# Kernel optimization log

Measured on AMD Instinct MI355X. Metric: run time of the kernel, lower is better.

## Reference

```python
import jax, jax.numpy as jnp
import numpy as np

KS = (7, 7)
ST = (3, 3)
PD = (3, 3)
DIM = 512
HID = 1960  # 40 * 49, divisible by kernel_shape


def _patch_flat_idx(out_h, out_w):
    kh, kw = KS; sh, sw = ST; ph, pw = PD
    oh = (out_h + 2 * ph - kh) // sh + 1
    ow = (out_w + 2 * pw - kw) // sw + 1
    Wp = out_w + 2 * pw
    iy = jnp.arange(kh)[:, None, None, None] + (jnp.arange(oh) * sh)[None, None, :, None]
    ix = jnp.arange(kw)[None, :, None, None] + (jnp.arange(ow) * sw)[None, None, None, :]
    # (kh, kw, oh, ow) flat index into padded image
    return (iy * Wp + ix), oh, ow


def fold(patches, out_h, out_w):
    # patches: (B, C*kh*kw, L) -> (B, C, out_h, out_w), overlap-add like F.fold
    kh, kw = KS; ph, pw = PD
    idx, oh, ow = _patch_flat_idx(out_h, out_w)
    B, CK, L = patches.shape
    C = CK // (kh * kw)
    Hp, Wp = out_h + 2 * ph, out_w + 2 * pw
    p = patches.reshape(B, C, kh, kw, oh, ow)
    out = jnp.zeros((B, C, Hp * Wp), patches.dtype)
    out = out.at[:, :, idx.reshape(-1)].add(p.reshape(B, C, -1))
    return out.reshape(B, C, Hp, Wp)[:, :, ph:ph + out_h, pw:pw + out_w]


def unfold(img, out_h, out_w):
    # img: (B, C, H, W) -> (B, C*kh*kw, L), like F.unfold
    kh, kw = KS; ph, pw = PD
    idx, oh, ow = _patch_flat_idx(out_h, out_w)
    B, C = img.shape[:2]
    imgp = jnp.pad(img, ((0, 0), (0, 0), (ph, ph), (pw, pw)))
    flat = imgp.reshape(B, C, -1)
    g = flat[:, :, idx.reshape(-1)].reshape(B, C, kh, kw, oh, ow)
    return g.reshape(B, C * kh * kw, oh * ow)


def setup_inputs() -> dict:
    key = jax.random.key(0)
    k1, k2, k3, k4, k5 = jax.random.split(key, 5)
    x = jax.random.normal(k1, (2, 5760, DIM), dtype=jnp.float32)
    W1 = jax.random.normal(k2, (HID, DIM), dtype=jnp.float32) * 0.02
    b1 = jax.random.normal(k3, (HID,), dtype=jnp.float32) * 0.02
    W2 = jax.random.normal(k4, (DIM, HID), dtype=jnp.float32) * 0.02
    b2 = jax.random.normal(k5, (DIM,), dtype=jnp.float32) * 0.02
    return {"x": x, "W1": W1, "b1": b1, "W2": W2, "b2": b2, "out_h": 60, "out_w": 108}


def reference(x, W1, b1, W2, b2, out_h, out_w):
    kh, kw = KS; sh, sw = ST; ph, pw = PD
    oh = (out_h + 2 * ph - kh) // sh + 1
    ow = (out_w + 2 * pw - kw) // sw + 1
    n_vecs = oh * ow
    h = jnp.einsum('bnd,hd->bnh', x, W1) + b1          # (b, n, HID)
    b_, n, c = h.shape
    p = h.reshape(-1, n_vecs, c).transpose(0, 2, 1)     # (B', c, L)
    folded = fold(p, out_h, out_w)                      # (B', c//49, H, W)
    ones = jnp.ones((p.shape[0], kh * kw, n_vecs), h.dtype)
    norm = fold(ones, out_h, out_w)                     # (B', 1, H, W)
    y = unfold(folded / norm, out_h, out_w)             # (B', c, L)
    y = y.transpose(0, 2, 1).reshape(b_, n, c)
    out = jnp.einsum('bnh,dh->bnd', jax.nn.gelu(y, approximate=False), W2) + b2
    return out
```

## Files before the change

### kernel.cpp

```cpp
#include <hip/hip_runtime.h>
#include <cmath>

#define M_ROWS   11520
#define DIM      512
#define HID      1960
#define HIDP     2048
#define KP2      1984
#define OH       20
#define OW       36
#define LVEC     720
#define NCH      40
#define BPRIME   16

typedef unsigned short u16;
typedef __bf16 bf16x8 __attribute__((ext_vector_type(8)));
typedef float  f32x4  __attribute__((ext_vector_type(4)));
typedef unsigned short u16x8 __attribute__((ext_vector_type(8)));

__device__ __forceinline__ u16 f2bf(float f) {
    unsigned u = __float_as_uint(f);
    u += 0x7fffu + ((u >> 16) & 1u);
    return (u16)(u >> 16);
}
__device__ __forceinline__ float bf2f(u16 h) {
    return __uint_as_float(((unsigned)h) << 16);
}

__device__ __forceinline__ void gload_lds16(const void* g, void* l) {
    __builtin_amdgcn_global_load_lds(
        (const __attribute__((address_space(1))) void*)g,
        (__attribute__((address_space(3))) void*)l, 16, 0, 0);
}

#define CVT_XB   5760
#define CVT_W1B  1024
#define CVT_W2B  1024
#define CVT_Z    270
__global__ __launch_bounds__(256) void cvt_all(const float* __restrict__ x,
                                               const float* __restrict__ W1,
                                               const float* __restrict__ W2,
                                               u16* __restrict__ xb,
                                               u16* __restrict__ W1b,
                                               u16* __restrict__ W2b,
                                               u16* __restrict__ g2) {
    const int b = blockIdx.x;
    const int tid = threadIdx.x;
    ushort4 o;
    if (b < CVT_XB) {
        int i = (b * 256 + tid) * 4;
        float4 v = *(const float4*)(x + i);
        o.x = f2bf(v.x); o.y = f2bf(v.y); o.z = f2bf(v.z); o.w = f2bf(v.w);
        *(ushort4*)(xb + i) = o;
    } else if (b < CVT_XB + CVT_W1B) {
        int i = ((b - CVT_XB) * 256 + tid) * 4;
        if (i < HID * DIM) {
            float4 v = *(const float4*)(W1 + i);
            o.x = f2bf(v.x); o.y = f2bf(v.y); o.z = f2bf(v.z); o.w = f2bf(v.w);
        } else {
            o.x = o.y = o.z = o.w = 0;
        }
        *(ushort4*)(W1b + i) = o;
    } else if (b < CVT_XB + CVT_W1B + CVT_W2B) {
        int i = ((b - CVT_XB - CVT_W1B) * 256 + tid) * 4;
        int d = i / HIDP, c = i - d * HIDP;
        if (c < HID) {
            float4 v = *(const float4*)(W2 + (size_t)d * HID + c);
            o.x = f2bf(v.x); o.y = f2bf(v.y); o.z = f2bf(v.z); o.w = f2bf(v.w);
        } else {
            o.x = o.y = o.z = o.w = 0;
        }
        *(ushort4*)(W2b + i) = o;
    } else {
        int i = ((b - CVT_XB - CVT_W1B - CVT_W2B) * 256 + tid) * 4;
        int row = i / 24, c = i - row * 24;
        o.x = o.y = o.z = o.w = 0;
        *(ushort4*)(g2 + (size_t)row * HIDP + HID + c) = o;
    }
}

__global__ __launch_bounds__(1024, 8) void gemm1_k(const u16* __restrict__ A,
                                                   const u16* __restrict__ B,
                                                   const float* __restrict__ bias,
                                                   u16* __restrict__ C) {
    __shared__ u16 smem[128 * 136];
    u16* sA = smem;
    u16* sB = smem + 128 * 64;

    const int tid  = threadIdx.x;
    const int NB   = gridDim.x;
    const int v    = (blockIdx.x & 7) * (NB >> 3) + (blockIdx.x >> 3);
    const int bm   = v >> 4;
    const int bn   = v & 15;
    const int lane = tid & 63;
    const int wv   = tid >> 6;
    const int wm   = (wv >> 2) * 32;
    const int wn   = (wv & 3) * 32;
    const int r    = lane & 15;
    const int quad = lane >> 4;

    const size_t Arow0 = (size_t)bm * 128 * DIM;
    const size_t Brow0 = (size_t)bn * 128 * DIM;

    const int srow = tid >> 3;
    const int scg  = (tid & 7) ^ (srow & 7);

    f32x4 acc[2][2] = {};

    for (int kt = 0; kt < DIM; kt += 64) {
        __syncthreads();
        gload_lds16(A + Arow0 + (size_t)srow * DIM + kt + scg * 8, (char*)sA + tid * 16);
        gload_lds16(B + Brow0 + (size_t)srow * DIM + kt + scg * 8, (char*)sB + tid * 16);
        __syncthreads();
#pragma unroll
        for (int kk = 0; kk < 2; kk++) {
            bf16x8 af[2], bg[2];
#pragma unroll
            for (int m = 0; m < 2; m++) {
                int row = wm + m * 16 + r;
                int c   = (kk * 4 + quad) ^ (row & 7);
                af[m] = *(const bf16x8*)(sA + row * 64 + c * 8);
            }
#pragma unroll
            for (int u = 0; u < 2; u++) {
                int row = wn + u * 16 + r;
                int c   = (kk * 4 + quad) ^ (row & 7);
                bg[u] = *(const bf16x8*)(sB + row * 64 + c * 8);
            }
#pragma unroll
            for (int m = 0; m < 2; m++)
#pragma unroll
                for (int u = 0; u < 2; u++)
                    acc[m][u] = __builtin_amdgcn_mfma_f32_16x16x32_bf16(
                        af[m], bg[u], acc[m][u], 0, 0, 0);
        }
    }

    __syncthreads();
    const int gn0 = bn * 128;
#pragma unroll
    for (int u = 0; u < 2; u++) {
        int gnl = wn + u * 16 + r;
        int gng = gn0 + gnl;
        float bv = (gng < HID) ? bias[gng] : 0.0f;
#pragma unroll
        for (int m = 0; m < 2; m++) {
            int gml = wm + m * 16 + quad * 4;
#pragma unroll
            for (int q = 0; q < 4; q++)
                smem[(gml + q) * 136 + gnl] = f2bf(acc[m][u][q] + bv);
        }
    }
    __syncthreads();
    const int row = tid >> 3;
    const int seg = tid & 7;
    const u16* src = smem + row * 136 + seg * 16;
    u16* dst = C + (size_t)(bm * 128 + row) * HIDP + gn0 + seg * 16;
    *(u16x8*)dst       = *(const u16x8*)src;
    *(u16x8*)(dst + 8) = *(const u16x8*)(src + 8);
}

__global__ __launch_bounds__(512, 8) void gemm2_k(const u16* __restrict__ A,
                                                  const u16* __restrict__ B,
                                                  const float* __restrict__ bias,
                                                  float* __restrict__ C) {
    __shared__ u16 sA[128 * 64];
    __shared__ u16 sB[64 * 64];

    const int tid  = threadIdx.x;
    const int NB   = gridDim.x;
    const int v    = (blockIdx.x & 7) * (NB >> 3) + (blockIdx.x >> 3);
    const int bm   = v >> 3;
    const int bn   = v & 7;
    const int lane = tid & 63;
    const int wv   = tid >> 6;
    const int wm   = (wv >> 1) * 32;
    const int wn   = (wv & 1) * 32;
    const int r    = lane & 15;
    const int quad = lane >> 4;

    const size_t Arow0 = (size_t)bm * 128 * HIDP;
    const size_t Brow0 = (size_t)bn * 64 * HIDP;

    f32x4 acc[2][2] = {};

    for (int kt = 0; kt < KP2; kt += 64) {
        __syncthreads();
#pragma unroll
        for (int i = 0; i < 2; i++) {
            int e   = i * 512 + tid;
            int row = e >> 3;
            int cg  = (e & 7) ^ (row & 7);
            gload_lds16(A + Arow0 + (size_t)row * HIDP + kt + cg * 8, (char*)sA + e * 16);
        }
        {
            int row = tid >> 3;
            int cg  = (tid & 7) ^ (row & 7);
            gload_lds16(B + Brow0 + (size_t)row * HIDP + kt + cg * 8, (char*)sB + tid * 16);
        }
        __syncthreads();
#pragma unroll
        for (int kk = 0; kk < 2; kk++) {
            bf16x8 af[2], bg[2];
#pragma unroll
            for (int m = 0; m < 2; m++) {
                int row = wm + m * 16 + r;
                int c   = (kk * 4 + quad) ^ (row & 7);
                af[m] = *(const bf16x8*)(sA + row * 64 + c * 8);
            }
#pragma unroll
            for (int u = 0; u < 2; u++) {
                int row = wn + u * 16 + r;
                int c   = (kk * 4 + quad) ^ (row & 7);
                bg[u] = *(const bf16x8*)(sB + row * 64 + c * 8);
            }
#pragma unroll
            for (int m = 0; m < 2; m++)
#pragma unroll
                for (int u = 0; u < 2; u++)
                    acc[m][u] = __builtin_amdgcn_mfma_f32_16x16x32_bf16(
                        af[m], bg[u], acc[m][u], 0, 0, 0);
        }
    }

    const int gm0 = bm * 128 + wm;
    const int gn0 = bn * 64 + wn;
#pragma unroll
    for (int u = 0; u < 2; u++) {
        int gn = gn0 + u * 16 + r;
        float bv = bias[gn];
#pragma unroll
        for (int m = 0; m < 2; m++) {
            int gm = gm0 + m * 16 + quad * 4;
#pragma unroll
            for (int q = 0; q < 4; q++)
                C[(size_t)(gm + q) * DIM + gn] = acc[m][u][q] + bv;
        }
    }
}

__global__ __launch_bounds__(512) void mid_fused(const u16* __restrict__ hg,
                                                 u16* __restrict__ g2) {
    __shared__ u16 sh[12 * 20 * 56];
    __shared__ u16 sG[34 * 58];

    const int b   = blockIdx.x;
    const int bp  = b / (NCH * 4);
    const int rr  = b - bp * (NCH * 4);
    const int ch  = rr >> 2;
    const int s   = (rr >> 1) & 1;
    const int xh  = rr & 1;
    const int o0  = s * 10;
    const int lo  = s * 8;
    const int ox0 = xh * 16;
    const int n0  = bp * LVEC;
    const int c0  = ch * 49;
    const int c0f = c0 & ~7;
    const int koff = c0 & 7;
    const int tid = threadIdx.x;

    {
        const char* hb = (const char*)(hg + (size_t)(n0 + lo * 36 + ox0) * HIDP + c0f);
        for (int t = tid; t < 12 * 20 * 7; t += 512) {
            int r   = (int)(((unsigned)t * 74899u) >> 19);
            int c   = t - r * 7;
            int loy = (int)(((unsigned)r * 3277u) >> 16);
            int oxl = r - 20 * loy;
            gload_lds16(hb + (size_t)(loy * 36 + oxl) * (HIDP * 2) + c * 16,
                        (char*)sh + t * 16);
        }
    }
    __syncthreads();

    const int pxl = tid & 63;
    const int rg  = tid >> 6;
    if (pxl < 58) {
        const int  pxg  = pxl + 54 * xh;
        const bool pxin = (pxg >= 3) && (pxg <= 110);
        const int  kx0  = pxg % 3;
        int  ct[3];
        bool vx[3];
        int  cx = 0;
#pragma unroll
        for (int dx = 0; dx < 3; dx++) {
            int kx = kx0 + 3 * dx, rx = pxg - kx;
            bool ok = pxin && (kx <= 6) && (rx >= 0) && (rx <= 105);
            vx[dx] = ok;
            ct[dx] = ok ? ((rx / 3) - ox0) * 56 + kx : 0;
            cx += ok ? 1 : 0;
        }
        const float fcx = (cx == 3) ? (1.0f / 3.0f) : ((cx == 2) ? 0.5f : 1.0f);

        for (int pr = rg; pr < 34; pr += 8) {
            int py = 3 * o0 + pr;
            float val = 0.0f;
            if (pxin && py >= 3 && py <= 62) {
                int ky0 = py % 3;
                float sum = 0.0f;
                int cy = 0;
#pragma unroll
                for (int dy = 0; dy < 3; dy++) {
                    int ky = ky0 + 3 * dy, ry = py - ky;
                    if (ky <= 6 && ry >= 0 && ry <= 57) {
                        int rt = (ry / 3 - lo) * (20 * 56) + ky * 7 + koff;
                        cy++;
                        float v0 = bf2f(sh[rt + ct[0]]);
                        float v1 = bf2f(sh[rt + ct[1]]);
                        float v2 = bf2f(sh[rt + ct[2]]);
                        sum += vx[0] ? v0 : 0.0f;
                        sum += vx[1] ? v1 : 0.0f;
                        sum += vx[2] ? v2 : 0.0f;
                    }
                }
                float fcy = (cy == 3) ? (1.0f / 3.0f) : ((cy == 2) ? 0.5f : 1.0f);
                float m = sum * fcx * fcy;
                val = 0.5f * m * (1.0f + erff(m * 0.70710678118654752f));
            }
            sG[pr * 58 + pxl] = f2bf(val);
        }
    }
    __syncthreads();

    {
        u16* g2row = g2 + (size_t)(n0 + o0 * 36 + 18 * xh) * HIDP + c0;
        for (int j = tid; j < 10 * 18 * 49; j += 512) {
            int l2 = (int)(((unsigned)j * 42800u) >> 21);
            int k  = j - l2 * 49;
            int oy = (int)(((unsigned)l2 * 57u) >> 10);
            int ox = l2 - 18 * oy;
            int ky = (int)(((unsigned)k * 37u) >> 8);
            int kx = k - 7 * ky;
            g2row[(size_t)(oy * 36 + ox) * HIDP + k] =
                sG[(3 * oy + ky) * 58 + 3 * ox + kx];
        }
    }
}

extern "C" void kernel_launch(void* const* d_in, const int* in_sizes, int n_in,
                              void* d_out, int out_size, void* d_ws, size_t ws_size,
                              hipStream_t stream) {
    (void)in_sizes; (void)n_in; (void)out_size; (void)ws_size;
    const float* x  = (const float*)d_in[0];
    const float* W1 = (const float*)d_in[1];
    const float* b1 = (const float*)d_in[2];
    const float* W2 = (const float*)d_in[3];
    const float* b2 = (const float*)d_in[4];
    float* out = (float*)d_out;

    char* ws = (char*)d_ws;
    u16* xb  = (u16*)(ws);
    u16* W1b = (u16*)(ws + 11796480);
    u16* W2b = (u16*)(ws + 13893632);
    u16* hg  = (u16*)(ws + 15990784);
    u16* g2  = (u16*)(ws + 63176704);

    cvt_all<<<CVT_XB + CVT_W1B + CVT_W2B + CVT_Z, 256, 0, stream>>>(
        x, W1, W2, xb, W1b, W2b, g2);

    gemm1_k<<<(M_ROWS / 128) * (HIDP / 128), 1024, 0, stream>>>(xb, W1b, b1, hg);

    mid_fused<<<BPRIME * NCH * 4, 512, 0, stream>>>(hg, g2);

    gemm2_k<<<(M_ROWS / 128) * (DIM / 64), 512, 0, stream>>>(g2, W2b, b2, out);
}
```

Before: 193.6 us.

## Rewrite gemm1 with 256x128 tiles and double-buffered LDS pipelining

Rewrites the first GEMM kernel to use 256x128 output tiles with 512 threads. Each wave now accumulates 8x2 MFMA tiles, and the global-to-LDS loads are double-buffered and staggered across sub-steps, using explicit vmcnt waits, raw s_barrier and setprio around the MFMA bursts. The aim is to overlap global loads with matrix math and to raise arithmetic intensity per LDS byte. In exchange it uses more registers and LDS per block and gives lower occupancy. The second GEMM is only renamed.

```diff
diff --git a/kernel.cpp b/kernel.cpp
--- a/kernel.cpp
+++ b/kernel.cpp
@@ -30,6 +30,12 @@
     __builtin_amdgcn_global_load_lds(
         (const __attribute__((address_space(1))) void*)g,
         (__attribute__((address_space(3))) void*)l, 16, 0, 0);
+}
+
+__device__ __forceinline__ void wg_barrier() {
+    asm volatile("" ::: "memory");
+    __builtin_amdgcn_s_barrier();
+    asm volatile("" ::: "memory");
 }
 
 #define CVT_XB   5760
@@ -78,13 +84,13 @@
     }
 }
 
-__global__ __launch_bounds__(1024, 8) void gemm1_k(const u16* __restrict__ A,
+__global__ __launch_bounds__(512, 2) void gemm1_8p(const u16* __restrict__ A,
                                                    const u16* __restrict__ B,
                                                    const float* __restrict__ bias,
                                                    u16* __restrict__ C) {
-    __shared__ u16 smem[128 * 136];
-    u16* sA = smem;
-    u16* sB = smem + 128 * 64;
+    constexpr int BUFU = (256 + 128) * 64;
+    constexpr int NT   = DIM / 64;
+    __shared__ u16 smem[2 * BUFU];
 
     const int tid  = threadIdx.x;
     const int NB   = gridDim.x;
@@ -93,76 +99,120 @@
     const int bn   = v & 15;
     const int lane = tid & 63;
     const int wv   = tid >> 6;
-    const int wm   = (wv >> 2) * 32;
-    const int wn   = (wv & 3) * 32;
+    const int wr   = wv >> 2;
+    const int wc   = wv & 3;
     const int r    = lane & 15;
     const int quad = lane >> 4;
 
-    const size_t Arow0 = (size_t)bm * 128 * DIM;
-    const size_t Brow0 = (size_t)bn * 128 * DIM;
-
-    const int srow = tid >> 3;
-    const int scg  = (tid & 7) ^ (srow & 7);
-
-    f32x4 acc[2][2] = {};
-
-    for (int kt = 0; kt < DIM; kt += 64) {
-        __syncthreads();
-        gload_lds16(A + Arow0 + (size_t)srow * DIM + kt + scg * 8, (char*)sA + tid * 16);
-        gload_lds16(B + Brow0 + (size_t)srow * DIM + kt + scg * 8, (char*)sB + tid * 16);
-        __syncthreads();
-#pragma unroll
-        for (int kk = 0; kk < 2; kk++) {
-            bf16x8 af[2], bg[2];
-#pragma unroll
-            for (int m = 0; m < 2; m++) {
-                int row = wm + m * 16 + r;
-                int c   = (kk * 4 + quad) ^ (row & 7);
-                af[m] = *(const bf16x8*)(sA + row * 64 + c * 8);
-            }
-#pragma unroll
-            for (int u = 0; u < 2; u++) {
-                int row = wn + u * 16 + r;
-                int c   = (kk * 4 + quad) ^ (row & 7);
-                bg[u] = *(const bf16x8*)(sB + row * 64 + c * 8);
-            }
-#pragma unroll
-            for (int m = 0; m < 2; m++)
-#pragma unroll
-                for (int u = 0; u < 2; u++)
-                    acc[m][u] = __builtin_amdgcn_mfma_f32_16x16x32_bf16(
-                        af[m], bg[u], acc[m][u], 0, 0, 0);
-        }
-    }
-
-    __syncthreads();
+    const size_t Arow0 = (size_t)bm * 256;
+    const size_t Brow0 = (size_t)bn * 128;
+
+    const int srl = tid >> 3;
+    const int scp = tid & 7;
+    auto stA = [&](int b2, int kt, int R0) {
+        int rl = R0 + srl;
+        int cg = scp ^ (rl & 7);
+        gload_lds16(A + (Arow0 + rl) * DIM + kt + cg * 8,
+                    (char*)(smem + b2 * BUFU) + R0 * 128 + tid * 16);
+    };
+    auto stB = [&](int b2, int kt, int R0) {
+        int rl = R0 + srl;
+        int cg = scp ^ (rl & 7);
+        gload_lds16(B + (Brow0 + rl) * DIM + kt + cg * 8,
+                    (char*)(smem + b2 * BUFU + 256 * 64) + R0 * 128 + tid * 16);
+    };
+
+    stB(0,  0, 0);  stB(0,  0, 64);
+    stA(0,  0, 0);  stA(0,  0, 128);
+    stA(0,  0, 64); stA(0,  0, 192);
+    stB(1, 64, 0);  stB(1, 64, 64);
+    stA(1, 64, 0);  stA(1, 64, 128);
+    asm volatile("s_waitcnt vmcnt(4)" ::: "memory");
+    wg_barrier();
+
+    f32x4 acc[8][2] = {};
+    bf16x8 bg[2][2];
+
+    for (int T = 0; T < NT; ++T) {
+        const int b = T & 1;
+        const u16* sAb = smem + b * BUFU;
+        const u16* sBb = sAb + 256 * 64;
+#pragma unroll
+        for (int q = 0; q < 4; ++q) {
+            bf16x8 af[2][2];
+#pragma unroll
+            for (int m2 = 0; m2 < 2; m2++) {
+                int row = wr * 128 + (2 * q + m2) * 16 + r;
+#pragma unroll
+                for (int kk = 0; kk < 2; kk++) {
+                    int c = (kk * 4 + quad) ^ (row & 7);
+                    af[m2][kk] = *(const bf16x8*)(sAb + row * 64 + c * 8);
+                }
+            }
+            if (q == 0) {
+#pragma unroll
+                for (int n = 0; n < 2; n++) {
+                    int row = wc * 32 + n * 16 + r;
+#pragma unroll
+                    for (int kk = 0; kk < 2; kk++) {
+                        int c = (kk * 4 + quad) ^ (row & 7);
+                        bg[n][kk] = *(const bf16x8*)(sBb + row * 64 + c * 8);
+                    }
+                }
+                if (T + 1 < NT) { stA(1 - b, (T + 1) * 64, 64); stA(1 - b, (T + 1) * 64, 192); }
+            } else if (q == 1) {
+                if (T + 2 < NT) { stB(b, (T + 2) * 64, 0); stB(b, (T + 2) * 64, 64); }
+            } else if (q == 2) {
+                if (T + 2 < NT) { stA(b, (T + 2) * 64, 0); stA(b, (T + 2) * 64, 128); }
+            }
+            wg_barrier();
+            __builtin_amdgcn_s_setprio(1);
+#pragma unroll
+            for (int m2 = 0; m2 < 2; m2++)
+#pragma unroll
+                for (int n = 0; n < 2; n++)
+#pragma unroll
+                    for (int kk = 0; kk < 2; kk++)
+                        acc[2 * q + m2][n] = __builtin_amdgcn_mfma_f32_16x16x32_bf16(
+                            af[m2][kk], bg[n][kk], acc[2 * q + m2][n], 0, 0, 0);
+            __builtin_amdgcn_s_setprio(0);
+            if (q == 3) {
+                if (T + 2 < NT)      asm volatile("s_waitcnt vmcnt(4)" ::: "memory");
+                else if (T + 1 < NT) asm volatile("s_waitcnt vmcnt(0)" ::: "memory");
+            }
+            wg_barrier();
+        }
+    }
+
     const int gn0 = bn * 128;
 #pragma unroll
-    for (int u = 0; u < 2; u++) {
-        int gnl = wn + u * 16 + r;
+    for (int n = 0; n < 2; n++) {
+        int gnl = wc * 32 + n * 16 + r;
         int gng = gn0 + gnl;
         float bv = (gng < HID) ? bias[gng] : 0.0f;
 #pragma unroll
-        for (int m = 0; m < 2; m++) {
-            int gml = wm + m * 16 + quad * 4;
-#pragma unroll
-            for (int q = 0; q < 4; q++)
-                smem[(gml + q) * 136 + gnl] = f2bf(acc[m][u][q] + bv);
-        }
-    }
-    __syncthreads();
-    const int row = tid >> 3;
-    const int seg = tid & 7;
-    const u16* src = smem + row * 136 + seg * 16;
-    u16* dst = C + (size_t)(bm * 128 + row) * HIDP + gn0 + seg * 16;
-    *(u16x8*)dst       = *(const u16x8*)src;
-    *(u16x8*)(dst + 8) = *(const u16x8*)(src + 8);
-}
-
-__global__ __launch_bounds__(512, 8) void gemm2_k(const u16* __restrict__ A,
-                                                  const u16* __restrict__ B,
-                                                  const float* __restrict__ bias,
-                                                  float* __restrict__ C) {
+        for (int m = 0; m < 8; m++) {
+            int gml = wr * 128 + m * 16 + quad * 4;
+#pragma unroll
+            for (int qq = 0; qq < 4; qq++)
+                smem[(gml + qq) * 136 + gnl] = f2bf(acc[m][n][qq] + bv);
+        }
+    }
+    asm volatile("s_waitcnt lgkmcnt(0)" ::: "memory");
+    wg_barrier();
+    const int row  = tid >> 1;
+    const int half = tid & 1;
+    const u16* src = smem + row * 136 + half * 64;
+    u16* dst = C + (size_t)(bm * 256 + row) * HIDP + gn0 + half * 64;
+#pragma unroll
+    for (int j = 0; j < 8; j++)
+        *(u16x8*)(dst + j * 8) = *(const u16x8*)(src + j * 8);
+}
+
+__global__ __launch_bounds__(512) void gemm2_bt(const u16* __restrict__ A,
+                                                const u16* __restrict__ B,
+                                                const float* __restrict__ bias,
+                                                float* __restrict__ C) {
     __shared__ u16 sA[128 * 64];
     __shared__ u16 sB[64 * 64];
 
@@ -356,9 +406,9 @@
     cvt_all<<<CVT_XB + CVT_W1B + CVT_W2B + CVT_Z, 256, 0, stream>>>(
         x, W1, W2, xb, W1b, W2b, g2);
 
-    gemm1_k<<<(M_ROWS / 128) * (HIDP / 128), 1024, 0, stream>>>(xb, W1b, b1, hg);
+    gemm1_8p<<<(M_ROWS / 256) * (HIDP / 128), 512, 0, stream>>>(xb, W1b, b1, hg);
 
     mid_fused<<<BPRIME * NCH * 4, 512, 0, stream>>>(hg, g2);
 
-    gemm2_k<<<(M_ROWS / 128) * (DIM / 64), 512, 0, stream>>>(g2, W2b, b2, out);
-}
+    gemm2_bt<<<(M_ROWS / 128) * (DIM / 64), 512, 0, stream>>>(g2, W2b, b2, out);
+}
```

New measurement: 205.1 us. 1.06x slower.

## Retile gemm1 to 128x64 blocks with 256 threads and direct stores

Applied to the files above, without the earlier changes.

Replaces the 1024-thread 128x128 gemm1 tile with a 256-thread 128x64 tile, where each wave computes a 32x64 sub-tile with 8 accumulators instead of 4. The LDS-staged coalesced epilogue is dropped and results are written straight to global memory. The grid doubles and LDS per block shrinks, which should allow more blocks per CU and more MFMA work per fragment load. In exchange, the direct scattered 2-byte stores may coalesce poorly. gemm2 is only renamed and its launch bound hint changes.

```diff
diff --git a/kernel.cpp b/kernel.cpp
--- a/kernel.cpp
+++ b/kernel.cpp
@@ -15,7 +15,6 @@
 typedef unsigned short u16;
 typedef __bf16 bf16x8 __attribute__((ext_vector_type(8)));
 typedef float  f32x4  __attribute__((ext_vector_type(4)));
-typedef unsigned short u16x8 __attribute__((ext_vector_type(8)));
 
 __device__ __forceinline__ u16 f2bf(float f) {
     unsigned u = __float_as_uint(f);
@@ -78,91 +77,90 @@
     }
 }
 
-__global__ __launch_bounds__(1024, 8) void gemm1_k(const u16* __restrict__ A,
-                                                   const u16* __restrict__ B,
-                                                   const float* __restrict__ bias,
-                                                   u16* __restrict__ C) {
-    __shared__ u16 smem[128 * 136];
-    u16* sA = smem;
-    u16* sB = smem + 128 * 64;
+__global__ __launch_bounds__(256) void gemm1_sm(const u16* __restrict__ A,
+                                                const u16* __restrict__ B,
+                                                const float* __restrict__ bias,
+                                                u16* __restrict__ C) {
+    __shared__ u16 sA[128 * 64];
+    __shared__ u16 sB[64 * 64];
 
     const int tid  = threadIdx.x;
     const int NB   = gridDim.x;
     const int v    = (blockIdx.x & 7) * (NB >> 3) + (blockIdx.x >> 3);
-    const int bm   = v >> 4;
-    const int bn   = v & 15;
+    const int bm   = v >> 5;
+    const int bn   = v & 31;
     const int lane = tid & 63;
     const int wv   = tid >> 6;
-    const int wm   = (wv >> 2) * 32;
-    const int wn   = (wv & 3) * 32;
+    const int wm   = wv * 32;
     const int r    = lane & 15;
     const int quad = lane >> 4;
 
     const size_t Arow0 = (size_t)bm * 128 * DIM;
-    const size_t Brow0 = (size_t)bn * 128 * DIM;
-
-    const int srow = tid >> 3;
-    const int scg  = (tid & 7) ^ (srow & 7);
-
-    f32x4 acc[2][2] = {};
+    const size_t Brow0 = (size_t)bn * 64 * DIM;
+
+    f32x4 acc[2][4] = {};
 
     for (int kt = 0; kt < DIM; kt += 64) {
         __syncthreads();
-        gload_lds16(A + Arow0 + (size_t)srow * DIM + kt + scg * 8, (char*)sA + tid * 16);
-        gload_lds16(B + Brow0 + (size_t)srow * DIM + kt + scg * 8, (char*)sB + tid * 16);
+#pragma unroll
+        for (int i = 0; i < 4; i++) {
+            int e   = i * 256 + tid;
+            int row = e >> 3;
+            int cg  = (e & 7) ^ (row & 7);
+            gload_lds16(A + Arow0 + (size_t)row * DIM + kt + cg * 8, (char*)sA + e * 16);
+        }
+#pragma unroll
+        for (int i = 0; i < 2; i++) {
+            int e   = i * 256 + tid;
+            int row = e >> 3;
+            int cg  = (e & 7) ^ (row & 7);
+            gload_lds16(B + Brow0 + (size_t)row * DIM + kt + cg * 8, (char*)sB + e * 16);
+        }
         __syncthreads();
 #pragma unroll
         for (int kk = 0; kk < 2; kk++) {
-            bf16x8 af[2], bg[2];
-#pragma unroll
-            for (int m = 0; m < 2; m++) {
-                int row = wm + m * 16 + r;
+            bf16x8 af[2], bg[4];
+#pragma unroll
+            for (int t = 0; t < 2; t++) {
+                int row = wm + t * 16 + r;
                 int c   = (kk * 4 + quad) ^ (row & 7);
-                af[m] = *(const bf16x8*)(sA + row * 64 + c * 8);
-            }
-#pragma unroll
-            for (int u = 0; u < 2; u++) {
-                int row = wn + u * 16 + r;
+                af[t] = *(const bf16x8*)(sA + row * 64 + c * 8);
+            }
+#pragma unroll
+            for (int u = 0; u < 4; u++) {
+                int row = u * 16 + r;
                 int c   = (kk * 4 + quad) ^ (row & 7);
                 bg[u] = *(const bf16x8*)(sB + row * 64 + c * 8);
             }
 #pragma unroll
-            for (int m = 0; m < 2; m++)
-#pragma unroll
-                for (int u = 0; u < 2; u++)
-                    acc[m][u] = __builtin_amdgcn_mfma_f32_16x16x32_bf16(
-                        af[m], bg[u], acc[m][u], 0, 0, 0);
-        }
-    }
-
-    __syncthreads();
-    const int gn0 = bn * 128;
-#pragma unroll
-    for (int u = 0; u < 2; u++) {
-        int gnl = wn + u * 16 + r;
-        int gng = gn0 + gnl;
-        float bv = (gng < HID) ? bias[gng] : 0.0f;
-#pragma unroll
-        for (int m = 0; m < 2; m++) {
-            int gml = wm + m * 16 + quad * 4;
+            for (int t = 0; t < 2; t++)
+#pragma unroll
+                for (int u = 0; u < 4; u++)
+                    acc[t][u] = __builtin_amdgcn_mfma_f32_16x16x32_bf16(
+                        af[t], bg[u], acc[t][u], 0, 0, 0);
+        }
+    }
+
+    const int gm0 = bm * 128 + wm;
+    const int gn0 = bn * 64;
+#pragma unroll
+    for (int u = 0; u < 4; u++) {
+        int gn = gn0 + u * 16 + r;
+        float bv = (gn < HID) ? bias[gn] : 0.0f;
+#pragma unroll
+        for (int t = 0; t < 2; t++) {
+            int gm = gm0 + t * 16 + quad * 4;
 #pragma unroll
             for (int q = 0; q < 4; q++)
-                smem[(gml + q) * 136 + gnl] = f2bf(acc[m][u][q] + bv);
-        }
-    }
-    __syncthreads();
-    const int row = tid >> 3;
-    const int seg = tid & 7;
-    const u16* src = smem + row * 136 + seg * 16;
-    u16* dst = C + (size_t)(bm * 128 + row) * HIDP + gn0 + seg * 16;
-    *(u16x8*)dst       = *(const u16x8*)src;
-    *(u16x8*)(dst + 8) = *(const u16x8*)(src + 8);
-}
-
-__global__ __launch_bounds__(512, 8) void gemm2_k(const u16* __restrict__ A,
-                                                  const u16* __restrict__ B,
-                                                  const float* __restrict__ bias,
-                                                  float* __restrict__ C) {
+                C[(size_t)(gm + q) * HIDP + gn] = f2bf(acc[t][u][q] + bv);
+        }
+    }
+}
+
+__global__ __launch_bounds__(512) void gemm2_bt(const u16* __restrict__ A,
+                                                const u16* __restrict__ B,
+                                                const float* __restrict__ bias,
+                                                float* __restrict__ C) {
     __shared__ u16 sA[128 * 64];
     __shared__ u16 sB[64 * 64];
 
@@ -356,9 +354,9 @@
     cvt_all<<<CVT_XB + CVT_W1B + CVT_W2B + CVT_Z, 256, 0, stream>>>(
         x, W1, W2, xb, W1b, W2b, g2);
 
-    gemm1_k<<<(M_ROWS / 128) * (HIDP / 128), 1024, 0, stream>>>(xb, W1b, b1, hg);
+    gemm1_sm<<<(M_ROWS / 128) * (HIDP / 64), 256, 0, stream>>>(xb, W1b, b1, hg);
 
     mid_fused<<<BPRIME * NCH * 4, 512, 0, stream>>>(hg, g2);
 
-    gemm2_k<<<(M_ROWS / 128) * (DIM / 64), 512, 0, stream>>>(g2, W2b, b2, out);
-}
+    gemm2_bt<<<(M_ROWS / 128) * (DIM / 64), 512, 0, stream>>>(g2, W2b, b2, out);
+}
```

Result: faster. 187.5 us (-3.1%).
